# Kernel optimization log

Hardware: AMD Instinct MI355X
Metric: run time of the kernel (lower is better)

The kernel has to match this reference:

```python
import jax, jax.numpy as jnp
import numpy as np

N = 100000
IN_CH = 128
OUT_CH = 128
H = 8
C = OUT_CH // H  # 16
K = 27  # kernel volume = 3**3
M = 1600000
BN_EPS = 1e-5


def _bn(x, gamma, beta):
    # training-mode BatchNorm1d over batch dim (biased variance)
    mu = x.mean(axis=0)
    var = x.var(axis=0)
    return (x - mu) * jax.lax.rsqrt(var + BN_EPS) * gamma + beta


def _l2norm(x):
    n = jnp.sqrt(jnp.sum(x * x, axis=-1, keepdims=True))
    return x / jnp.maximum(n, 1e-12)


def setup_inputs() -> dict:
    key = jax.random.key(0)
    ks = jax.random.split(key, 24)
    feats = jax.random.normal(ks[0], (N, IN_CH), jnp.float32)
    points = jax.random.normal(ks[1], (N, 3), jnp.float32)
    key_idx = jax.random.randint(ks[2], (M,), 0, N)
    kern_idx = jax.random.randint(ks[3], (M,), 0, K)
    q_idx = jax.random.randint(ks[4], (M,), 0, N)
    kq_map = jnp.stack([key_idx * K + kern_idx, q_idx]).astype(jnp.int32)
    s = 0.05
    params = dict(
        W1=jax.random.normal(ks[5], (3, 3), jnp.float32) * s,
        g1=jnp.ones((3,), jnp.float32), b1=jnp.zeros((3,), jnp.float32),
        W2=jax.random.normal(ks[6], (3, IN_CH), jnp.float32) * s,
        g2=jnp.ones((IN_CH,), jnp.float32), b2=jnp.zeros((IN_CH,), jnp.float32),
        W3=jax.random.normal(ks[7], (IN_CH, IN_CH), jnp.float32) * s,
        b3=jnp.zeros((IN_CH,), jnp.float32),
        Wq=jax.random.normal(ks[8], (IN_CH, OUT_CH), jnp.float32) * s,
        bq=jnp.zeros((OUT_CH,), jnp.float32),
        Wv=jax.random.normal(ks[9], (IN_CH, OUT_CH), jnp.float32) * s,
        bv=jnp.zeros((OUT_CH,), jnp.float32),
        pos_enc=jax.random.normal(ks[10], (K, H, C), jnp.float32),
        Wo=jax.random.normal(ks[11], (OUT_CH, OUT_CH), jnp.float32) * s,
        bo=jnp.zeros((OUT_CH,), jnp.float32),
    )
    return dict(feats=feats, points=points, kq_map=kq_map, **params)


def reference(feats, points, kq_map, W1, g1, b1, W2, g2, b2, W3, b3,
              Wq, bq, Wv, bv, pos_enc, Wo, bo):
    # intra-voxel positional MLP
    h = jax.nn.relu(_bn(points @ W1, g1, b1))
    h = jax.nn.relu(_bn(h @ W2, g2, b2))
    intra = h @ W3 + b3
    x = feats + intra  # [N, in_ch]
    q = (x @ Wq + bq).reshape(N, H, C)
    v = (x @ Wv + bv).reshape(N, H, C)
    nq = _l2norm(q)
    npe = _l2norm(pos_enc)  # [K, H, C]
    kern_idx = kq_map[0] % K
    key_idx = kq_map[0] // K
    q_idx = kq_map[1]
    # cosine-sim scores per map entry: [M, H]
    attn = jnp.einsum('mhc,mhc->mh', nq[q_idx], npe[kern_idx])
    # scatter weighted values to queries
    msg = attn[:, :, None] * v[key_idx]  # [M, H, C]
    out = jax.ops.segment_sum(msg, q_idx, num_segments=N)  # [N, H, C]
    out = out.reshape(N, OUT_CH) @ Wo + bo
    return out
```

## Files before the change

### kernel.cpp

```cpp
#include <hip/hip_runtime.h>
#include <hip/hip_bf16.h>
#include <stdint.h>


typedef unsigned short u16;
typedef __attribute__((ext_vector_type(8))) u16 u16x8;
typedef __attribute__((ext_vector_type(8))) short short8;
typedef __attribute__((ext_vector_type(4))) float f32x4;

#define CH 128
#define KVOL 27
#define CAP 64
#define LSTR 136
#define BN_EPS 1e-5f

__device__ __forceinline__ float bits2f(u16 u) {
  return __uint_as_float(((unsigned int)u) << 16);
}
__device__ __forceinline__ u16 f2bits(float x) {
  __hip_bfloat16 h = __float2bfloat16(x);
  return *reinterpret_cast<u16*>(&h);
}
__device__ __forceinline__ float ldf(const void* p, int i, bool bf) {
  return bf ? bits2f(((const u16*)p)[i]) : ((const float*)p)[i];
}
template <bool BF16>
__device__ __forceinline__ float ld(const void* p, int i) {
  if (BF16) return bits2f(((const u16*)p)[i]);
  return ((const float*)p)[i];
}

__global__ void detect_kernel(const void* g1, int* flag) {
  if (threadIdx.x == 0) flag[0] = (((const unsigned*)g1)[0] == 0x3F803F80u) ? 1 : 0;
}

__global__ void prep_all(const void* W3, const void* Wq, const void* Wv, const void* Wo,
                         const void* b3, const void* bq, const void* bv, const void* bo,
                         const void* pos_enc,
                         u16* W3T, u16* WqT, u16* WvT, u16* WoT,
                         float* b3f, float* bqf, float* bvf, float* bof,
                         float* npe, const int* flag) {
  bool bf = (*flag != 0);
  int bid = blockIdx.x, t = threadIdx.x;
  if (bid < 256) {
    int idx = bid * 256 + t;
    int sel = idx >> 14;
    int r = idx & (CH * CH - 1);
    int k = r >> 7, n = r & 127;
    const void* src = (sel == 0) ? W3 : (sel == 1) ? Wq : (sel == 2) ? Wv : Wo;
    u16*       dst = (sel == 0) ? W3T : (sel == 1) ? WqT : (sel == 2) ? WvT : WoT;
    dst[n * CH + k] = f2bits(ldf(src, k * CH + n, bf));
  } else if (bid == 256) {
    for (int idx = t; idx < 4 * CH; idx += 256) {
      int which = idx >> 7, j = idx & 127;
      const void* src = (which == 0) ? b3 : (which == 1) ? bq : (which == 2) ? bv : bo;
      float* dst = (which == 0) ? b3f : (which == 1) ? bqf : (which == 2) ? bvf : bof;
      dst[j] = ldf(src, j, bf);
    }
  } else {
    int k = bid - 257;
    if (t < CH) {
      float val = ldf(pos_enc, k * CH + t, bf);
      float ss = val * val;
      ss += __shfl_xor(ss, 1); ss += __shfl_xor(ss, 2);
      ss += __shfl_xor(ss, 4); ss += __shfl_xor(ss, 8);
      npe[k * CH + t] = val / fmaxf(sqrtf(ss), 1e-12f);
    }
  }
}

template <bool BF16>
__device__ void stats1_body(const void* points, const void* W1, float* stats1, int N,
                            float red[4][6]) {
  float w[9];
#pragma unroll
  for (int i = 0; i < 9; i++) w[i] = ld<BF16>(W1, i);
  float s[3] = {0.f, 0.f, 0.f}, ss[3] = {0.f, 0.f, 0.f};
  for (int p = blockIdx.x * blockDim.x + threadIdx.x; p < N; p += gridDim.x * blockDim.x) {
    float a0 = ld<BF16>(points, p * 3 + 0);
    float a1 = ld<BF16>(points, p * 3 + 1);
    float a2 = ld<BF16>(points, p * 3 + 2);
#pragma unroll
    for (int i = 0; i < 3; i++) {
      float v = a0 * w[i] + a1 * w[3 + i] + a2 * w[6 + i];
      s[i] += v; ss[i] += v * v;
    }
  }
#pragma unroll
  for (int i = 0; i < 3; i++) {
    for (int off = 32; off; off >>= 1) {
      s[i] += __shfl_down(s[i], off);
      ss[i] += __shfl_down(ss[i], off);
    }
  }
  int wave = threadIdx.x >> 6;
  if ((threadIdx.x & 63) == 0) {
#pragma unroll
    for (int i = 0; i < 3; i++) { red[wave][i] = s[i]; red[wave][3 + i] = ss[i]; }
  }
  __syncthreads();
  if (threadIdx.x == 0) {
#pragma unroll
    for (int i = 0; i < 6; i++) {
      float acc = red[0][i] + red[1][i] + red[2][i] + red[3][i];
      atomicAdd(&stats1[i], acc);
    }
  }
}
__global__ void stats1_kernel(const void* points, const void* W1, float* stats1, int N,
                              const int* flag) {
  __shared__ float red[4][6];
  if (*flag) stats1_body<true>(points, W1, stats1, N, red);
  else       stats1_body<false>(points, W1, stats1, N, red);
}

template <bool BF16>
__device__ void stats2a_body(const void* points, const void* W1, const void* g1,
                             const void* b1, const void* W2, const float* stats1,
                             float* partials, int N, float sh_s[2][CH], float sh_q[2][CH]) {
  int j = threadIdx.x & 127, psub = threadIdx.x >> 7;
  float w1[9];
#pragma unroll
  for (int i = 0; i < 9; i++) w1[i] = ld<BF16>(W1, i);
  float invN = 1.0f / (float)N;
  float s1[3], o1[3];
#pragma unroll
  for (int i = 0; i < 3; i++) {
    float mu = stats1[i] * invN;
    float var = stats1[3 + i] * invN - mu * mu;
    float sc = ld<BF16>(g1, i) * rsqrtf(var + BN_EPS);
    s1[i] = sc; o1[i] = ld<BF16>(b1, i) - mu * sc;
  }
  float w2c[3];
#pragma unroll
  for (int a = 0; a < 3; a++) w2c[a] = ld<BF16>(W2, a * CH + j);
  float sum = 0.f, ssum = 0.f;
  for (int p = blockIdx.x * 2 + psub; p < N; p += gridDim.x * 2) {
    float a0 = ld<BF16>(points, p * 3 + 0);
    float a1 = ld<BF16>(points, p * 3 + 1);
    float a2 = ld<BF16>(points, p * 3 + 2);
    float h2 = 0.f;
#pragma unroll
    for (int i = 0; i < 3; i++) {
      float p1 = a0 * w1[i] + a1 * w1[3 + i] + a2 * w1[6 + i];
      float h1 = fmaxf(p1 * s1[i] + o1[i], 0.f);
      h2 += h1 * w2c[i];
    }
    sum += h2; ssum += h2 * h2;
  }
  sh_s[psub][j] = sum; sh_q[psub][j] = ssum;
  __syncthreads();
  if (psub == 0) {
    partials[blockIdx.x * 256 + j] = sum + sh_s[1][j];
    partials[blockIdx.x * 256 + 128 + j] = ssum + sh_q[1][j];
  }
}
__global__ void stats2a_kernel(const void* points, const void* W1, const void* g1,
                               const void* b1, const void* W2, const float* stats1,
                               float* partials, int N, const int* flag) {
  __shared__ float sh_s[2][CH], sh_q[2][CH];
  if (*flag) stats2a_body<true>(points, W1, g1, b1, W2, stats1, partials, N, sh_s, sh_q);
  else       stats2a_body<false>(points, W1, g1, b1, W2, stats1, partials, N, sh_s, sh_q);
}
__global__ void stats2b_kernel(const float* __restrict__ partials, float* __restrict__ st2,
                               int B) {
  __shared__ float red[256];
  int t = blockIdx.x;
  int i = threadIdx.x;
  float a = 0.f;
  for (int b = i; b < B; b += 256) a += partials[(size_t)b * 256 + t];
  red[i] = a;
  __syncthreads();
  for (int off = 128; off; off >>= 1) {
    if (i < off) red[i] += red[i + off];
    __syncthreads();
  }
  if (i == 0) st2[t] = red[0];
}

__device__ __forceinline__ void gemm_core128(const u16* sA, const u16* sB,
                                             f32x4 acc[2][8], int wave, int lane) {
  int q = lane >> 4, r = lane & 15;
  int rowA0 = (wave * 32 + r) * LSTR;
  int rowA1 = (wave * 32 + 16 + r) * LSTR;
#pragma unroll
  for (int ks = 0; ks < 4; ks++) {
    int kk = ks * 32 + q * 8;
    short8 a0 = *(const short8*)&sA[rowA0 + kk];
    short8 a1 = *(const short8*)&sA[rowA1 + kk];
#pragma unroll
    for (int c = 0; c < 8; c++) {
      short8 b = *(const short8*)&sB[(c * 16 + r) * LSTR + kk];
      acc[0][c] = __builtin_amdgcn_mfma_f32_16x16x32_bf16(a0, b, acc[0][c], 0, 0, 0);
      acc[1][c] = __builtin_amdgcn_mfma_f32_16x16x32_bf16(a1, b, acc[1][c], 0, 0, 0);
    }
  }
}
__device__ __forceinline__ void stage_w(const u16* Wg, u16* sB, int tid) {
  for (int chk = tid; chk < 2048; chk += 256) {
    int n = chk >> 4, c = chk & 15;
    *(u16x8*)&sB[n * LSTR + c * 8] = *(const u16x8*)&Wg[n * CH + c * 8];
  }
}
__device__ __forceinline__ void zero_acc(f32x4 acc[2][8]) {
#pragma unroll
  for (int wm = 0; wm < 2; wm++)
#pragma unroll
    for (int c = 0; c < 8; c++) acc[wm][c] = (f32x4){0.f, 0.f, 0.f, 0.f};
}
__device__ __forceinline__ void cvals_to_lds(const f32x4 acc[2][8], const float* bias,
                                             u16* dst, int wave, int q, int r) {
#pragma unroll
  for (int wm = 0; wm < 2; wm++) {
#pragma unroll
    for (int c = 0; c < 8; c++) {
      int col = c * 16 + r;
      float bj = bias[col];
#pragma unroll
      for (int i = 0; i < 4; i++) {
        int lrow = wave * 32 + wm * 16 + q * 4 + i;
        dst[lrow * LSTR + col] = f2bits(acc[wm][c][i] + bj);
      }
    }
  }
}

__global__ __launch_bounds__(256)
void fused_qv_kernel(const void* points, const void* feats,
                     const void* W1, const void* g1, const void* b1,
                     const void* W2, const void* g2, const void* b2,
                     const u16* W3T, const u16* WqT, const u16* WvT,
                     const float* b3f, const float* bqf, const float* bvf,
                     const float* st1, const float* st2,
                     u16* nq16, u16* v16, int N, const int* flag) {
  __shared__ __align__(16) u16 sA[128 * LSTR];
  __shared__ __align__(16) u16 sB[128 * LSTR];
  __shared__ float s_pts[128 * 3];
  bool bf = (*flag != 0);
  int tid = threadIdx.x;
  int m0 = blockIdx.x * 128;
  int lane = tid & 63, wave = tid >> 6;
  int q = lane >> 4, r = lane & 15;

  for (int idx = tid; idx < 128 * 3; idx += 256) {
    int g = m0 * 3 + idx;
    s_pts[idx] = (g < N * 3) ? ldf(points, g, bf) : 0.f;
  }
  stage_w(W3T, sB, tid);
  __syncthreads();

  {
    int j = tid & 127, psub = tid >> 7;
    float w1[9];
#pragma unroll
    for (int i = 0; i < 9; i++) w1[i] = ldf(W1, i, bf);
    float invN = 1.0f / (float)N;
    float s1[3], o1[3];
#pragma unroll
    for (int i = 0; i < 3; i++) {
      float mu = st1[i] * invN;
      float var = st1[3 + i] * invN - mu * mu;
      float sc = ldf(g1, i, bf) * rsqrtf(var + BN_EPS);
      s1[i] = sc; o1[i] = ldf(b1, i, bf) - mu * sc;
    }
    float w2c[3];
#pragma unroll
    for (int a = 0; a < 3; a++) w2c[a] = ldf(W2, a * CH + j, bf);
    float mu2 = st2[j] * invN;
    float var2 = st2[CH + j] * invN - mu2 * mu2;
    float s2 = ldf(g2, j, bf) * rsqrtf(var2 + BN_EPS);
    float o2 = ldf(b2, j, bf) - mu2 * s2;
#pragma unroll 4
    for (int e = 0; e < 64; e++) {
      int m = psub + e * 2;
      float a0 = s_pts[m * 3 + 0];
      float a1 = s_pts[m * 3 + 1];
      float a2 = s_pts[m * 3 + 2];
      float h2 = 0.f;
#pragma unroll
      for (int i = 0; i < 3; i++) {
        float p1 = a0 * w1[i] + a1 * w1[3 + i] + a2 * w1[6 + i];
        float h1 = fmaxf(p1 * s1[i] + o1[i], 0.f);
        h2 += h1 * w2c[i];
      }
      sA[m * LSTR + j] = f2bits(fmaxf(h2 * s2 + o2, 0.f));
    }
  }
  __syncthreads();

  f32x4 acc[2][8];
  zero_acc(acc);
  gemm_core128(sA, sB, acc, wave, lane);
  cvals_to_lds(acc, b3f, sA, wave, q, r);
  __syncthreads();
  for (int chk = tid; chk < 2048; chk += 256) {
    int m = chk >> 4, c = chk & 15;
    int grow = m0 + m;
    if (grow < N) {
      u16x8 xv = *(const u16x8*)&sA[m * LSTR + c * 8];
      float fv[8];
      if (bf) {
        u16x8 fw = *(const u16x8*)((const u16*)feats + (size_t)grow * CH + c * 8);
#pragma unroll
        for (int k = 0; k < 8; k++) fv[k] = bits2f(fw[k]);
      } else {
        const float* fp = (const float*)feats + (size_t)grow * CH + c * 8;
        f32x4 f0 = *(const f32x4*)fp;
        f32x4 f1 = *(const f32x4*)(fp + 4);
#pragma unroll
        for (int k = 0; k < 4; k++) { fv[k] = f0[k]; fv[4 + k] = f1[k]; }
      }
      u16x8 outv;
#pragma unroll
      for (int k = 0; k < 8; k++) outv[k] = f2bits(bits2f(xv[k]) + fv[k]);
      *(u16x8*)&sA[m * LSTR + c * 8] = outv;
    }
  }
  stage_w(WqT, sB, tid);
  __syncthreads();

  zero_acc(acc);
  gemm_core128(sA, sB, acc, wave, lane);
  float nvals[2][8][4];
#pragma unroll
  for (int wm = 0; wm < 2; wm++) {
#pragma unroll
    for (int c = 0; c < 8; c++) {
      float bj = bqf[c * 16 + r];
#pragma unroll
      for (int i = 0; i < 4; i++) {
        float v = acc[wm][c][i] + bj;
        float ss = v * v;
        ss += __shfl_xor(ss, 1); ss += __shfl_xor(ss, 2);
        ss += __shfl_xor(ss, 4); ss += __shfl_xor(ss, 8);
        nvals[wm][c][i] = v / fmaxf(sqrtf(ss), 1e-12f);
      }
    }
  }
  __syncthreads();
#pragma unroll
  for (int wm = 0; wm < 2; wm++)
#pragma unroll
    for (int c = 0; c < 8; c++)
#pragma unroll
      for (int i = 0; i < 4; i++) {
        int lrow = wave * 32 + wm * 16 + q * 4 + i;
        sB[lrow * LSTR + c * 16 + r] = f2bits(nvals[wm][c][i]);
      }
  __syncthreads();
  for (int chk = tid; chk < 2048; chk += 256) {
    int m = chk >> 4, c = chk & 15;
    int grow = m0 + m;
    if (grow < N)
      *(u16x8*)&nq16[(size_t)grow * CH + c * 8] = *(const u16x8*)&sB[m * LSTR + c * 8];
  }
  __syncthreads();
  stage_w(WvT, sB, tid);
  __syncthreads();

  zero_acc(acc);
  gemm_core128(sA, sB, acc, wave, lane);
  __syncthreads();
  cvals_to_lds(acc, bvf, sB, wave, q, r);
  __syncthreads();
  for (int chk = tid; chk < 2048; chk += 256) {
    int m = chk >> 4, c = chk & 15;
    int grow = m0 + m;
    if (grow < N)
      *(u16x8*)&v16[(size_t)grow * CH + c * 8] = *(const u16x8*)&sB[m * LSTR + c * 8];
  }
}

__global__ __launch_bounds__(256)
void gemm_out_kernel(const u16* __restrict__ A, const u16* __restrict__ WoT,
                     const float* __restrict__ bof, void* __restrict__ out,
                     int N, const int* flag) {
  __shared__ __align__(16) u16 sA[128 * LSTR];
  __shared__ __align__(16) u16 sB[128 * LSTR];
  bool bf = (*flag != 0);
  int tid = threadIdx.x;
  int m0 = blockIdx.x * 128;
  int lane = tid & 63, wave = tid >> 6;
  int q = lane >> 4, r = lane & 15;
  stage_w(WoT, sB, tid);
  for (int chk = tid; chk < 2048; chk += 256) {
    int m = chk >> 4, c = chk & 15;
    int gm = m0 + m;
    u16x8 val = {0, 0, 0, 0, 0, 0, 0, 0};
    if (gm < N) val = *(const u16x8*)&A[(size_t)gm * CH + c * 8];
    *(u16x8*)&sA[m * LSTR + c * 8] = val;
  }
  __syncthreads();
  f32x4 acc[2][8];
  zero_acc(acc);
  gemm_core128(sA, sB, acc, wave, lane);
  __syncthreads();
  cvals_to_lds(acc, bof, sB, wave, q, r);
  __syncthreads();
  for (int chk = tid; chk < 2048; chk += 256) {
    int m = chk >> 4, c = chk & 15;
    int grow = m0 + m;
    if (grow < N) {
      u16x8 v = *(const u16x8*)&sB[m * LSTR + c * 8];
      if (bf) {
        *(u16x8*)((u16*)out + (size_t)grow * CH + c * 8) = v;
      } else {
        float* op = (float*)out + (size_t)grow * CH + c * 8;
        f32x4 f0, f1;
#pragma unroll
        for (int k = 0; k < 4; k++) { f0[k] = bits2f(v[k]); f1[k] = bits2f(v[4 + k]); }
        *(f32x4*)op = f0;
        *(f32x4*)(op + 4) = f1;
      }
    }
  }
}

__global__ void fill_kernel(const int* __restrict__ kq0, const int* __restrict__ kq1,
                            int* __restrict__ counts, int* __restrict__ bucket,
                            int M, int N) {
  int g = blockIdx.x & 7;
  int qlo = (int)(((long long)N * g) >> 3);
  int qhi = (int)(((long long)N * (g + 1)) >> 3);
  int nb = gridDim.x >> 3;
  int ib = blockIdx.x >> 3;
  int stride = nb * blockDim.x;
  for (int m = ib * blockDim.x + threadIdx.x; m < M; m += stride) {
    int q = kq1[m];
    if (q >= qlo && q < qhi) {
      int c0 = kq0[m];
      int pos = atomicAdd(&counts[q], 1);
      if (pos < CAP) bucket[(size_t)q * CAP + pos] = c0;
    }
  }
}

__global__ void attn_kernel(const float* __restrict__ npe, const u16* __restrict__ nq16,
                            const u16* __restrict__ v16, const int* __restrict__ counts,
                            const int* __restrict__ bucket, u16* __restrict__ segsum) {
  __shared__ float s_nq[CH];
  __shared__ float s_sc[CAP][8];
  __shared__ int s_key[CAP], s_e[CAP];
  __shared__ float s_par[2][CH];
  int n = blockIdx.x, t = threadIdx.x;
  int cnt = counts[n];
  cnt = (cnt > CAP) ? CAP : cnt;
  if (t < cnt) {
    int c0 = bucket[(size_t)n * CAP + t];
    int key = c0 / KVOL;
    s_key[t] = key;
    s_e[t] = c0 - key * KVOL;
  }
  s_nq[t] = bits2f(nq16[n * CH + t]);
  __syncthreads();
  int tot = cnt << 3;
  for (int base = 0; base < tot; base += 128) {
    int idx = base + t;
    if (idx < tot) {
      int i = idx >> 3, h = idx & 7;
      const float* pe = &npe[s_e[i] * CH + h * 16];
      const float* nn = &s_nq[h * 16];
      float s = 0.f;
#pragma unroll
      for (int cc = 0; cc < 16; cc += 4) {
        f32x4 p = *(const f32x4*)(pe + cc);
        f32x4 nv = *(const f32x4*)(nn + cc);
#pragma unroll
        for (int k = 0; k < 4; k++) s = fmaf(nv[k], p[k], s);
      }
      s_sc[i][h] = s;
    }
  }
  __syncthreads();
  int w = t >> 6, l = t & 63;
  int h = l >> 3;
  float a0 = 0.f, a1 = 0.f;
  int i = w;
  for (; i + 6 < cnt; i += 8) {
    unsigned g0 = *(const unsigned*)&v16[(size_t)s_key[i] * CH + 2 * l];
    unsigned g1 = *(const unsigned*)&v16[(size_t)s_key[i + 2] * CH + 2 * l];
    unsigned g2 = *(const unsigned*)&v16[(size_t)s_key[i + 4] * CH + 2 * l];
    unsigned g3 = *(const unsigned*)&v16[(size_t)s_key[i + 6] * CH + 2 * l];
    float sc0 = s_sc[i][h], sc1 = s_sc[i + 2][h];
    float sc2 = s_sc[i + 4][h], sc3 = s_sc[i + 6][h];
    a0 = fmaf(sc0, bits2f((u16)(g0 & 0xffff)), a0);
    a1 = fmaf(sc0, bits2f((u16)(g0 >> 16)), a1);
    a0 = fmaf(sc1, bits2f((u16)(g1 & 0xffff)), a0);
    a1 = fmaf(sc1, bits2f((u16)(g1 >> 16)), a1);
    a0 = fmaf(sc2, bits2f((u16)(g2 & 0xffff)), a0);
    a1 = fmaf(sc2, bits2f((u16)(g2 >> 16)), a1);
    a0 = fmaf(sc3, bits2f((u16)(g3 & 0xffff)), a0);
    a1 = fmaf(sc3, bits2f((u16)(g3 >> 16)), a1);
  }
  for (; i < cnt; i += 2) {
    unsigned g0 = *(const unsigned*)&v16[(size_t)s_key[i] * CH + 2 * l];
    float sc0 = s_sc[i][h];
    a0 = fmaf(sc0, bits2f((u16)(g0 & 0xffff)), a0);
    a1 = fmaf(sc0, bits2f((u16)(g0 >> 16)), a1);
  }
  s_par[w][2 * l] = a0;
  s_par[w][2 * l + 1] = a1;
  __syncthreads();
  if (t < 64) {
    float r0 = s_par[0][2 * t] + s_par[1][2 * t];
    float r1 = s_par[0][2 * t + 1] + s_par[1][2 * t + 1];
    unsigned o = (unsigned)f2bits(r0) | ((unsigned)f2bits(r1) << 16);
    *(unsigned*)&segsum[(size_t)n * CH + 2 * t] = o;
  }
}

extern "C" void kernel_launch(void* const* d_in, const int* in_sizes, int n_in,
                              void* d_out, int out_size, void* d_ws, size_t ws_size,
                              hipStream_t stream) {
  const void* feats   = d_in[0];
  const void* points  = d_in[1];
  const int*  kq      = (const int*)d_in[2];
  const void* W1      = d_in[3];
  const void* g1      = d_in[4];
  const void* b1      = d_in[5];
  const void* W2      = d_in[6];
  const void* g2      = d_in[7];
  const void* b2      = d_in[8];
  const void* W3      = d_in[9];
  const void* b3      = d_in[10];
  const void* Wq      = d_in[11];
  const void* bq      = d_in[12];
  const void* Wv      = d_in[13];
  const void* bv      = d_in[14];
  const void* pos_enc = d_in[15];
  const void* Wo      = d_in[16];
  const void* bo      = d_in[17];

  const int N = in_sizes[0] / CH;
  const int M = in_sizes[2] / 2;
  const int* kq0 = kq;
  const int* kq1 = kq + M;

  char* ws = (char*)d_ws;
  size_t off = 0;
  auto alloc = [&](size_t bytes) -> void* {
    void* p = ws + off;
    off = (off + bytes + 255) & ~(size_t)255;
    return p;
  };
  const int SB = 2048;
  int*   flag    = (int*)alloc(sizeof(int));
  float* npe     = (float*)alloc(KVOL * CH * sizeof(float));
  u16*   W3T     = (u16*)alloc(CH * CH * sizeof(u16));
  u16*   WqT     = (u16*)alloc(CH * CH * sizeof(u16));
  u16*   WvT     = (u16*)alloc(CH * CH * sizeof(u16));
  u16*   WoT     = (u16*)alloc(CH * CH * sizeof(u16));
  float* b3f     = (float*)alloc(CH * sizeof(float));
  float* bqf     = (float*)alloc(CH * sizeof(float));
  float* bvf     = (float*)alloc(CH * sizeof(float));
  float* bof     = (float*)alloc(CH * sizeof(float));
  float* st1     = (float*)alloc(8 * sizeof(float));
  float* st2     = (float*)alloc(2 * CH * sizeof(float));
  float* part2   = (float*)alloc((size_t)SB * 256 * sizeof(float));
  u16*   nqbuf   = (u16*)alloc((size_t)N * CH * sizeof(u16));
  u16*   vbuf    = (u16*)alloc((size_t)N * CH * sizeof(u16));
  u16*   segbuf  = (u16*)alloc((size_t)N * CH * sizeof(u16));
  int*   counts  = (int*)alloc((size_t)N * sizeof(int));
  int*   bucket  = (int*)alloc((size_t)N * CAP * sizeof(int));

  hipMemsetAsync(st1, 0, 8 * sizeof(float), stream);
  hipMemsetAsync(counts, 0, (size_t)N * sizeof(int), stream);

  detect_kernel<<<1, 64, 0, stream>>>(g1, flag);
  prep_all<<<257 + KVOL, 256, 0, stream>>>(W3, Wq, Wv, Wo, b3, bq, bv, bo, pos_enc,
                                           W3T, WqT, WvT, WoT, b3f, bqf, bvf, bof,
                                           npe, flag);
  stats1_kernel<<<128, 256, 0, stream>>>(points, W1, st1, N, flag);
  stats2a_kernel<<<SB, 256, 0, stream>>>(points, W1, g1, b1, W2, st1, part2, N, flag);
  stats2b_kernel<<<256, 256, 0, stream>>>(part2, st2, SB);
  fill_kernel<<<1024, 256, 0, stream>>>(kq0, kq1, counts, bucket, M, N);

  int gblocks = (N + 127) / 128;
  fused_qv_kernel<<<gblocks, 256, 0, stream>>>(points, feats, W1, g1, b1, W2, g2, b2,
                                               W3T, WqT, WvT, b3f, bqf, bvf, st1, st2,
                                               nqbuf, vbuf, N, flag);
  attn_kernel<<<N, CH, 0, stream>>>(npe, nqbuf, vbuf, counts, bucket, segbuf);
  gemm_out_kernel<<<gblocks, 256, 0, stream>>>(segbuf, WoT, bof, d_out, N, flag);
}
```

Before: 439.4 us.

## Batch four queries per attention block and drop the dtype-detect kernel

The attention kernel now handles four query rows per 256-thread block instead of one row per 128-thread block. Each wave owns one query and accumulates all of its neighbours without a cross-wave reduction, and the gather loop is unrolled by eight. The separate detect kernel and flag buffer are removed: each kernel checks the g1 bit pattern inline, which saves one launch. The fill kernel's grid is doubled. The risk is load imbalance within a block when neighbour counts differ across the four queries.

```diff
diff --git a/kernel.cpp b/kernel.cpp
--- a/kernel.cpp
+++ b/kernel.cpp
@@ -29,18 +29,17 @@
   if (BF16) return bits2f(((const u16*)p)[i]);
   return ((const float*)p)[i];
 }
-
-__global__ void detect_kernel(const void* g1, int* flag) {
-  if (threadIdx.x == 0) flag[0] = (((const unsigned*)g1)[0] == 0x3F803F80u) ? 1 : 0;
+__device__ __forceinline__ bool is_bf16(const void* g1) {
+  return ((const unsigned*)g1)[0] == 0x3F803F80u;
 }
 
 __global__ void prep_all(const void* W3, const void* Wq, const void* Wv, const void* Wo,
                          const void* b3, const void* bq, const void* bv, const void* bo,
-                         const void* pos_enc,
+                         const void* pos_enc, const void* g1,
                          u16* W3T, u16* WqT, u16* WvT, u16* WoT,
                          float* b3f, float* bqf, float* bvf, float* bof,
-                         float* npe, const int* flag) {
-  bool bf = (*flag != 0);
+                         float* npe) {
+  bool bf = is_bf16(g1);
   int bid = blockIdx.x, t = threadIdx.x;
   if (bid < 256) {
     int idx = bid * 256 + t;
@@ -107,11 +106,11 @@
     }
   }
 }
-__global__ void stats1_kernel(const void* points, const void* W1, float* stats1, int N,
-                              const int* flag) {
+__global__ void stats1_kernel(const void* points, const void* W1, const void* g1,
+                              float* stats1, int N) {
   __shared__ float red[4][6];
-  if (*flag) stats1_body<true>(points, W1, stats1, N, red);
-  else       stats1_body<false>(points, W1, stats1, N, red);
+  if (is_bf16(g1)) stats1_body<true>(points, W1, stats1, N, red);
+  else             stats1_body<false>(points, W1, stats1, N, red);
 }
 
 template <bool BF16>
@@ -157,10 +156,10 @@
 }
 __global__ void stats2a_kernel(const void* points, const void* W1, const void* g1,
                                const void* b1, const void* W2, const float* stats1,
-                               float* partials, int N, const int* flag) {
+                               float* partials, int N) {
   __shared__ float sh_s[2][CH], sh_q[2][CH];
-  if (*flag) stats2a_body<true>(points, W1, g1, b1, W2, stats1, partials, N, sh_s, sh_q);
-  else       stats2a_body<false>(points, W1, g1, b1, W2, stats1, partials, N, sh_s, sh_q);
+  if (is_bf16(g1)) stats2a_body<true>(points, W1, g1, b1, W2, stats1, partials, N, sh_s, sh_q);
+  else             stats2a_body<false>(points, W1, g1, b1, W2, stats1, partials, N, sh_s, sh_q);
 }
 __global__ void stats2b_kernel(const float* __restrict__ partials, float* __restrict__ st2,
                                int B) {
@@ -232,11 +231,11 @@
                      const u16* W3T, const u16* WqT, const u16* WvT,
                      const float* b3f, const float* bqf, const float* bvf,
                      const float* st1, const float* st2,
-                     u16* nq16, u16* v16, int N, const int* flag) {
+                     u16* nq16, u16* v16, int N) {
   __shared__ __align__(16) u16 sA[128 * LSTR];
   __shared__ __align__(16) u16 sB[128 * LSTR];
   __shared__ float s_pts[128 * 3];
-  bool bf = (*flag != 0);
+  bool bf = is_bf16(g1);
   int tid = threadIdx.x;
   int m0 = blockIdx.x * 128;
   int lane = tid & 63, wave = tid >> 6;
@@ -373,11 +372,11 @@
 
 __global__ __launch_bounds__(256)
 void gemm_out_kernel(const u16* __restrict__ A, const u16* __restrict__ WoT,
-                     const float* __restrict__ bof, void* __restrict__ out,
-                     int N, const int* flag) {
+                     const float* __restrict__ bof, const void* g1,
+                     void* __restrict__ out, int N) {
   __shared__ __align__(16) u16 sA[128 * LSTR];
   __shared__ __align__(16) u16 sB[128 * LSTR];
-  bool bf = (*flag != 0);
+  bool bf = is_bf16(g1);
   int tid = threadIdx.x;
   int m0 = blockIdx.x * 128;
   int lane = tid & 63, wave = tid >> 6;
@@ -435,77 +434,110 @@
   }
 }
 
-__global__ void attn_kernel(const float* __restrict__ npe, const u16* __restrict__ nq16,
-                            const u16* __restrict__ v16, const int* __restrict__ counts,
-                            const int* __restrict__ bucket, u16* __restrict__ segsum) {
-  __shared__ float s_nq[CH];
-  __shared__ float s_sc[CAP][8];
-  __shared__ int s_key[CAP], s_e[CAP];
-  __shared__ float s_par[2][CH];
-  int n = blockIdx.x, t = threadIdx.x;
-  int cnt = counts[n];
-  cnt = (cnt > CAP) ? CAP : cnt;
-  if (t < cnt) {
-    int c0 = bucket[(size_t)n * CAP + t];
+__global__ __launch_bounds__(256)
+void attn_kernel(const float* __restrict__ npe, const u16* __restrict__ nq16,
+                 const u16* __restrict__ v16, const int* __restrict__ counts,
+                 const int* __restrict__ bucket, u16* __restrict__ segsum, int N) {
+  __shared__ float s_nq[4][CH];
+  __shared__ float s_sc[4][CAP][8];
+  __shared__ int s_key[4][CAP], s_e[4][CAP];
+  __shared__ int s_cnt[4];
+  int t = threadIdx.x;
+  int n0 = blockIdx.x * 4;
+  int qq = t >> 6, l = t & 63;
+  int n = n0 + qq;
+  int cnt = 0;
+  if (n < N) {
+    cnt = counts[n];
+    cnt = (cnt > CAP) ? CAP : cnt;
+  }
+  if (l == 0) s_cnt[qq] = cnt;
+  if (l < cnt) {
+    int c0 = bucket[(size_t)n * CAP + l];
     int key = c0 / KVOL;
-    s_key[t] = key;
-    s_e[t] = c0 - key * KVOL;
-  }
-  s_nq[t] = bits2f(nq16[n * CH + t]);
-  __syncthreads();
-  int tot = cnt << 3;
-  for (int base = 0; base < tot; base += 128) {
-    int idx = base + t;
-    if (idx < tot) {
-      int i = idx >> 3, h = idx & 7;
-      const float* pe = &npe[s_e[i] * CH + h * 16];
-      const float* nn = &s_nq[h * 16];
-      float s = 0.f;
-#pragma unroll
-      for (int cc = 0; cc < 16; cc += 4) {
-        f32x4 p = *(const f32x4*)(pe + cc);
-        f32x4 nv = *(const f32x4*)(nn + cc);
-#pragma unroll
-        for (int k = 0; k < 4; k++) s = fmaf(nv[k], p[k], s);
+    s_key[qq][l] = key;
+    s_e[qq][l] = c0 - key * KVOL;
+  }
+  {
+    unsigned g = (n < N) ? *(const unsigned*)&nq16[(size_t)n * CH + 2 * l] : 0u;
+    s_nq[qq][2 * l] = bits2f((u16)(g & 0xffff));
+    s_nq[qq][2 * l + 1] = bits2f((u16)(g >> 16));
+  }
+  __syncthreads();
+#pragma unroll
+  for (int q2 = 0; q2 < 4; q2++) {
+    int tot = s_cnt[q2] << 3;
+    for (int base = 0; base < tot; base += 256) {
+      int id2 = base + t;
+      if (id2 < tot) {
+        int i = id2 >> 3, h = id2 & 7;
+        const float* pe = &npe[s_e[q2][i] * CH + h * 16];
+        const float* nn = &s_nq[q2][h * 16];
+        float s = 0.f;
+#pragma unroll
+        for (int cc = 0; cc < 16; cc += 4) {
+          f32x4 p = *(const f32x4*)(pe + cc);
+          f32x4 nv = *(const f32x4*)(nn + cc);
+#pragma unroll
+          for (int k = 0; k < 4; k++) s = fmaf(nv[k], p[k], s);
+        }
+        s_sc[q2][i][h] = s;
       }
-      s_sc[i][h] = s;
-    }
-  }
-  __syncthreads();
-  int w = t >> 6, l = t & 63;
+    }
+  }
+  __syncthreads();
   int h = l >> 3;
   float a0 = 0.f, a1 = 0.f;
-  int i = w;
-  for (; i + 6 < cnt; i += 8) {
-    unsigned g0 = *(const unsigned*)&v16[(size_t)s_key[i] * CH + 2 * l];
-    unsigned g1 = *(const unsigned*)&v16[(size_t)s_key[i + 2] * CH + 2 * l];
-    unsigned g2 = *(const unsigned*)&v16[(size_t)s_key[i + 4] * CH + 2 * l];
-    unsigned g3 = *(const unsigned*)&v16[(size_t)s_key[i + 6] * CH + 2 * l];
-    float sc0 = s_sc[i][h], sc1 = s_sc[i + 2][h];
-    float sc2 = s_sc[i + 4][h], sc3 = s_sc[i + 6][h];
-    a0 = fmaf(sc0, bits2f((u16)(g0 & 0xffff)), a0);
-    a1 = fmaf(sc0, bits2f((u16)(g0 >> 16)), a1);
-    a0 = fmaf(sc1, bits2f((u16)(g1 & 0xffff)), a0);
-    a1 = fmaf(sc1, bits2f((u16)(g1 >> 16)), a1);
-    a0 = fmaf(sc2, bits2f((u16)(g2 & 0xffff)), a0);
-    a1 = fmaf(sc2, bits2f((u16)(g2 >> 16)), a1);
-    a0 = fmaf(sc3, bits2f((u16)(g3 & 0xffff)), a0);
-    a1 = fmaf(sc3, bits2f((u16)(g3 >> 16)), a1);
-  }
-  for (; i < cnt; i += 2) {
-    unsigned g0 = *(const unsigned*)&v16[(size_t)s_key[i] * CH + 2 * l];
-    float sc0 = s_sc[i][h];
-    a0 = fmaf(sc0, bits2f((u16)(g0 & 0xffff)), a0);
-    a1 = fmaf(sc0, bits2f((u16)(g0 >> 16)), a1);
-  }
-  s_par[w][2 * l] = a0;
-  s_par[w][2 * l + 1] = a1;
-  __syncthreads();
-  if (t < 64) {
-    float r0 = s_par[0][2 * t] + s_par[1][2 * t];
-    float r1 = s_par[0][2 * t + 1] + s_par[1][2 * t + 1];
-    unsigned o = (unsigned)f2bits(r0) | ((unsigned)f2bits(r1) << 16);
-    *(unsigned*)&segsum[(size_t)n * CH + 2 * t] = o;
+  const int* kq = s_key[qq];
+  int i = 0;
+  for (; i + 7 < cnt; i += 8) {
+    unsigned g0 = *(const unsigned*)&v16[(size_t)kq[i] * CH + 2 * l];
+    unsigned g1 = *(const unsigned*)&v16[(size_t)kq[i + 1] * CH + 2 * l];
+    unsigned g2 = *(const unsigned*)&v16[(size_t)kq[i + 2] * CH + 2 * l];
+    unsigned g3 = *(const unsigned*)&v16[(size_t)kq[i + 3] * CH + 2 * l];
+    unsigned g4 = *(const unsigned*)&v16[(size_t)kq[i + 4] * CH + 2 * l];
+    unsigned g5 = *(const unsigned*)&v16[(size_t)kq[i + 5] * CH + 2 * l];
+    unsigned g6 = *(const unsigned*)&v16[(size_t)kq[i + 6] * CH + 2 * l];
+    unsigned g7 = *(const unsigned*)&v16[(size_t)kq[i + 7] * CH + 2 * l];
+    float s0 = s_sc[qq][i][h],     s1 = s_sc[qq][i + 1][h];
+    float s2 = s_sc[qq][i + 2][h], s3 = s_sc[qq][i + 3][h];
+    float s4 = s_sc[qq][i + 4][h], s5 = s_sc[qq][i + 5][h];
+    float s6 = s_sc[qq][i + 6][h], s7 = s_sc[qq][i + 7][h];
+    a0 = fmaf(s0, bits2f((u16)(g0 & 0xffff)), a0);
+    a1 = fmaf(s0, bits2f((u16)(g0 >> 16)), a1);
+    a0 = fmaf(s1, bits2f((u16)(g1 & 0xffff)), a0);
+    a1 = fmaf(s1, bits2f((u16)(g1 >> 16)), a1);
+    a0 = fmaf(s2, bits2f((u16)(g2 & 0xffff)), a0);
+    a1 = fmaf(s2, bits2f((u16)(g2 >> 16)), a1);
+    a0 = fmaf(s3, bits2f((u16)(g3 & 0xffff)), a0);
+    a1 = fmaf(s3, bits2f((u16)(g3 >> 16)), a1);
+    a0 = fmaf(s4, bits2f((u16)(g4 & 0xffff)), a0);
+    a1 = fmaf(s4, bits2f((u16)(g4 >> 16)), a1);
+    a0 = fmaf(s5, bits2f((u16)(g5 & 0xffff)), a0);
+    a1 = fmaf(s5, bits2f((u16)(g5 >> 16)), a1);
+    a0 = fmaf(s6, bits2f((u16)(g6 & 0xffff)), a0);
+    a1 = fmaf(s6, bits2f((u16)(g6 >> 16)), a1);
+    a0 = fmaf(s7, bits2f((u16)(g7 & 0xffff)), a0);
+    a1 = fmaf(s7, bits2f((u16)(g7 >> 16)), a1);
+  }
+  for (; i + 1 < cnt; i += 2) {
+    unsigned g0 = *(const unsigned*)&v16[(size_t)kq[i] * CH + 2 * l];
+    unsigned g1 = *(const unsigned*)&v16[(size_t)kq[i + 1] * CH + 2 * l];
+    float s0 = s_sc[qq][i][h], s1 = s_sc[qq][i + 1][h];
+    a0 = fmaf(s0, bits2f((u16)(g0 & 0xffff)), a0);
+    a1 = fmaf(s0, bits2f((u16)(g0 >> 16)), a1);
+    a0 = fmaf(s1, bits2f((u16)(g1 & 0xffff)), a0);
+    a1 = fmaf(s1, bits2f((u16)(g1 >> 16)), a1);
+  }
+  if (i < cnt) {
+    unsigned g0 = *(const unsigned*)&v16[(size_t)kq[i] * CH + 2 * l];
+    float s0 = s_sc[qq][i][h];
+    a0 = fmaf(s0, bits2f((u16)(g0 & 0xffff)), a0);
+    a1 = fmaf(s0, bits2f((u16)(g0 >> 16)), a1);
+  }
+  if (n < N) {
+    unsigned o = (unsigned)f2bits(a0) | ((unsigned)f2bits(a1) << 16);
+    *(unsigned*)&segsum[(size_t)n * CH + 2 * l] = o;
   }
 }
 
@@ -544,7 +576,6 @@
     return p;
   };
   const int SB = 2048;
-  int*   flag    = (int*)alloc(sizeof(int));
   float* npe     = (float*)alloc(KVOL * CH * sizeof(float));
   u16*   W3T     = (u16*)alloc(CH * CH * sizeof(u16));
   u16*   WqT     = (u16*)alloc(CH * CH * sizeof(u16));
@@ -566,19 +597,18 @@
   hipMemsetAsync(st1, 0, 8 * sizeof(float), stream);
   hipMemsetAsync(counts, 0, (size_t)N * sizeof(int), stream);
 
-  detect_kernel<<<1, 64, 0, stream>>>(g1, flag);
-  prep_all<<<257 + KVOL, 256, 0, stream>>>(W3, Wq, Wv, Wo, b3, bq, bv, bo, pos_enc,
-                                           W3T, WqT, WvT, WoT, b3f, bqf, bvf, bof,
-                                           npe, flag);
-  stats1_kernel<<<128, 256, 0, stream>>>(points, W1, st1, N, flag);
-  stats2a_kernel<<<SB, 256, 0, stream>>>(points, W1, g1, b1, W2, st1, part2, N, flag);
+  prep_all<<<257 + KVOL, 256, 0, stream>>>(W3, Wq, Wv, Wo, b3, bq, bv, bo, pos_enc, g1,
+                                           W3T, WqT, WvT, WoT, b3f, bqf, bvf, bof, npe);
+  stats1_kernel<<<128, 256, 0, stream>>>(points, W1, g1, st1, N);
+  stats2a_kernel<<<SB, 256, 0, stream>>>(points, W1, g1, b1, W2, st1, part2, N);
   stats2b_kernel<<<256, 256, 0, stream>>>(part2, st2, SB);
-  fill_kernel<<<1024, 256, 0, stream>>>(kq0, kq1, counts, bucket, M, N);
+  fill_kernel<<<2048, 256, 0, stream>>>(kq0, kq1, counts, bucket, M, N);
 
   int gblocks = (N + 127) / 128;
   fused_qv_kernel<<<gblocks, 256, 0, stream>>>(points, feats, W1, g1, b1, W2, g2, b2,
                                                W3T, WqT, WvT, b3f, bqf, bvf, st1, st2,
-                                               nqbuf, vbuf, N, flag);
-  attn_kernel<<<N, CH, 0, stream>>>(npe, nqbuf, vbuf, counts, bucket, segbuf);
-  gemm_out_kernel<<<gblocks, 256, 0, stream>>>(segbuf, WoT, bof, d_out, N, flag);
-}
+                                               nqbuf, vbuf, N);
+  attn_kernel<<<(N + 3) / 4, 256, 0, stream>>>(npe, nqbuf, vbuf, counts, bucket,
+                                               segbuf, N);
+  gemm_out_kernel<<<gblocks, 256, 0, stream>>>(segbuf, WoT, bof, g1, d_out, N);
+}
```

New measurement: 416.7 us. 1.05x faster.
